# Optimization experiments

Hardware: AMD Instinct MI355X
Metric: run time of the kernel (lower is better)

Reference implementation:

```python
import jax, jax.numpy as jnp
import numpy as np

LPC_ORDER = 32
GAMMA = 1.0  # get_gamma(1, None) == 1


def setup_inputs() -> dict:
    key = jax.random.key(0)
    # PARCOR coefficients, magnitude < 1 for stability; shape (..., M+1)
    k = jax.random.uniform(key, (16, 65536, LPC_ORDER + 1), dtype=jnp.float32)
    return {"k": k}


def reference(k):
    # Levinson-style PARCOR -> LPC recursion (diffsptk par2lpc).
    # a starts as k / gamma; for m = 2..M: a[1:m] += k[m] * flip(a[1:m])
    M1 = k.shape[-1]
    a = k / GAMMA
    for m in range(2, M1):  # fixed, small unrolled loop over order
        km = k[..., m : m + 1]          # (..., 1)  reflection coefficient
        am = a[..., 1:m]                 # (..., m-1) current LPC prefix
        a = a.at[..., 1:m].set(am + km * am[..., ::-1])
    return a
```

## Files before the change

kernel.cpp:

```cpp
#include <hip/hip_runtime.h>

#define M1      33
#define TROWS   64
#define BLK     64
#define TILE_F  (TROWS * M1)
#define PARTIAL 16
#define GRID    2304

__global__ __launch_bounds__(BLK, 1)
void parcor_to_lpc_kernel(const float* __restrict__ k, float* __restrict__ out,
                          int ntiles) {
    __shared__ __align__(16) float lds[2 * TILE_F];
    const int lane = threadIdx.x;

    int tile = blockIdx.x;
    if (tile >= ntiles) return;
    const int stride = gridDim.x;

    float4 R0, R1, R2, R3, R4, R5, R6, R7, R8;

#define LOAD_TILE(gbase)  do {                                        \
        const float4* g4_ = (const float4*)(gbase);                   \
        R0 = g4_[0 * BLK + lane];  R1 = g4_[1 * BLK + lane];          \
        R2 = g4_[2 * BLK + lane];  R3 = g4_[3 * BLK + lane];          \
        R4 = g4_[4 * BLK + lane];  R5 = g4_[5 * BLK + lane];          \
        R6 = g4_[6 * BLK + lane];  R7 = g4_[7 * BLK + lane];          \
        if (lane < PARTIAL) R8 = g4_[8 * BLK + lane];                 \
    } while (0)

#define STAGE_TILE(lbase) do {                                        \
        float4* l4_ = (float4*)(lbase);                               \
        l4_[0 * BLK + lane] = R0;  l4_[1 * BLK + lane] = R1;          \
        l4_[2 * BLK + lane] = R2;  l4_[3 * BLK + lane] = R3;          \
        l4_[4 * BLK + lane] = R4;  l4_[5 * BLK + lane] = R5;          \
        l4_[6 * BLK + lane] = R6;  l4_[7 * BLK + lane] = R7;          \
        if (lane < PARTIAL) l4_[8 * BLK + lane] = R8;                 \
    } while (0)

    LOAD_TILE(k + (size_t)tile * TILE_F);
    STAGE_TILE(lds);

    int buf = 0;
    while (true) {
        const int next = tile + stride;

        if (next < ntiles)
            LOAD_TILE(k + (size_t)next * TILE_F);

        float* L = lds + buf * TILE_F;

        asm volatile("s_waitcnt lgkmcnt(0)" ::: "memory");

        float a[M1];
        #pragma unroll
        for (int j = 0; j < M1; ++j) a[j] = L[lane * M1 + j];

        #pragma unroll
        for (int m = 2; m < M1; ++m) {
            const float km = a[m];
            #pragma unroll
            for (int j = 1; 2 * j < m; ++j) {
                const float x = a[j];
                const float y = a[m - j];
                a[j]     = fmaf(km, y, x);
                a[m - j] = fmaf(km, x, y);
            }
            if ((m & 1) == 0) {
                const int j = m >> 1;
                a[j] = fmaf(km, a[j], a[j]);
            }
        }

        #pragma unroll
        for (int j = 0; j < M1; ++j) L[lane * M1 + j] = a[j];
        asm volatile("s_waitcnt lgkmcnt(0)" ::: "memory");

        {
            const float4* l4 = (const float4*)L;
            float4* g4o = (float4*)(out + (size_t)tile * TILE_F);
            #pragma unroll
            for (int i = 0; i < 8; ++i) g4o[i * BLK + lane] = l4[i * BLK + lane];
            if (lane < PARTIAL) g4o[8 * BLK + lane] = l4[8 * BLK + lane];
        }

        if (next >= ntiles) break;

        STAGE_TILE(lds + (buf ^ 1) * TILE_F);

        tile = next;
        buf ^= 1;
    }
#undef LOAD_TILE
#undef STAGE_TILE
}

__global__ void parcor_to_lpc_tail_kernel(const float* __restrict__ k,
                                          float* __restrict__ out,
                                          int row_start, int nrows) {
    const int row = row_start + blockIdx.x * blockDim.x + threadIdx.x;
    if (row >= nrows) return;
    const float* src = k + (size_t)row * M1;
    float* dst = out + (size_t)row * M1;
    float a[M1];
    #pragma unroll
    for (int j = 0; j < M1; ++j) a[j] = src[j];
    #pragma unroll
    for (int m = 2; m < M1; ++m) {
        const float km = a[m];
        #pragma unroll
        for (int j = 1; 2 * j < m; ++j) {
            const float x = a[j];
            const float y = a[m - j];
            a[j]     = fmaf(km, y, x);
            a[m - j] = fmaf(km, x, y);
        }
        if ((m & 1) == 0) {
            const int j = m >> 1;
            a[j] = fmaf(km, a[j], a[j]);
        }
    }
    #pragma unroll
    for (int j = 0; j < M1; ++j) dst[j] = a[j];
}

extern "C" void kernel_launch(void* const* d_in, const int* in_sizes, int n_in,
                              void* d_out, int out_size, void* d_ws, size_t ws_size,
                              hipStream_t stream) {
    const float* k = (const float*)d_in[0];
    float* out = (float*)d_out;

    const int nrows     = in_sizes[0] / M1;
    const int ntiles    = nrows / TROWS;
    const int tile_rows = ntiles * TROWS;
    const int rem       = nrows - tile_rows;

    if (ntiles > 0) {
        const int grid = ntiles < GRID ? ntiles : GRID;
        parcor_to_lpc_kernel<<<grid, BLK, 0, stream>>>(k, out, ntiles);
    }
    if (rem > 0)
        parcor_to_lpc_tail_kernel<<<(rem + 63) / 64, 64, 0, stream>>>(
            k, out, tile_rows, nrows);
}
```

Measured before the change: 242.8 us.

## Deepen prefetch to two register tile sets with single LDS buffer

Replaces the double-buffered LDS pipeline with two alternating register tile sets (A/B), so global loads are issued two tiles ahead instead of one, while using a single LDS tile buffer. The grid is also resized to 18 blocks per CU times 256. The intent is to keep more memory loads in flight per wave to hide HBM latency in this bandwidth-bound kernel. The cost is doubled register usage for prefetch data, which may lower occupancy or cause spills.

```diff
diff --git a/kernel.cpp b/kernel.cpp
--- a/kernel.cpp
+++ b/kernel.cpp
@@ -5,93 +5,100 @@
 #define BLK     64
 #define TILE_F  (TROWS * M1)
 #define PARTIAL 16
-#define GRID    2304
+#define BPC     18
+#define GRID    (BPC * 256)
 
 __global__ __launch_bounds__(BLK, 1)
 void parcor_to_lpc_kernel(const float* __restrict__ k, float* __restrict__ out,
                           int ntiles) {
-    __shared__ __align__(16) float lds[2 * TILE_F];
+    __shared__ __align__(16) float lds[TILE_F];
     const int lane = threadIdx.x;
 
-    int tile = blockIdx.x;
-    if (tile >= ntiles) return;
-    const int stride = gridDim.x;
+    int tA = blockIdx.x;
+    if (tA >= ntiles) return;
+    const int stride  = gridDim.x;
+    const int stride2 = 2 * stride;
 
-    float4 R0, R1, R2, R3, R4, R5, R6, R7, R8;
+    float4 A0, A1, A2, A3, A4, A5, A6, A7, A8;
+    float4 B0, B1, B2, B3, B4, B5, B6, B7, B8;
 
-#define LOAD_TILE(gbase)  do {                                        \
-        const float4* g4_ = (const float4*)(gbase);                   \
-        R0 = g4_[0 * BLK + lane];  R1 = g4_[1 * BLK + lane];          \
-        R2 = g4_[2 * BLK + lane];  R3 = g4_[3 * BLK + lane];          \
-        R4 = g4_[4 * BLK + lane];  R5 = g4_[5 * BLK + lane];          \
-        R6 = g4_[6 * BLK + lane];  R7 = g4_[7 * BLK + lane];          \
-        if (lane < PARTIAL) R8 = g4_[8 * BLK + lane];                 \
+#define LOADSET(P, gbase) do {                                          \
+        const float4* g4_ = (const float4*)(gbase);                     \
+        P##0 = g4_[0 * BLK + lane];  P##1 = g4_[1 * BLK + lane];        \
+        P##2 = g4_[2 * BLK + lane];  P##3 = g4_[3 * BLK + lane];        \
+        P##4 = g4_[4 * BLK + lane];  P##5 = g4_[5 * BLK + lane];        \
+        P##6 = g4_[6 * BLK + lane];  P##7 = g4_[7 * BLK + lane];        \
+        if (lane < PARTIAL) P##8 = g4_[8 * BLK + lane];                 \
     } while (0)
 
-#define STAGE_TILE(lbase) do {                                        \
-        float4* l4_ = (float4*)(lbase);                               \
-        l4_[0 * BLK + lane] = R0;  l4_[1 * BLK + lane] = R1;          \
-        l4_[2 * BLK + lane] = R2;  l4_[3 * BLK + lane] = R3;          \
-        l4_[4 * BLK + lane] = R4;  l4_[5 * BLK + lane] = R5;          \
-        l4_[6 * BLK + lane] = R6;  l4_[7 * BLK + lane] = R7;          \
-        if (lane < PARTIAL) l4_[8 * BLK + lane] = R8;                 \
+#define STAGESET(P) do {                                                \
+        float4* l4_ = (float4*)lds;                                     \
+        l4_[0 * BLK + lane] = P##0;  l4_[1 * BLK + lane] = P##1;        \
+        l4_[2 * BLK + lane] = P##2;  l4_[3 * BLK + lane] = P##3;        \
+        l4_[4 * BLK + lane] = P##4;  l4_[5 * BLK + lane] = P##5;        \
+        l4_[6 * BLK + lane] = P##6;  l4_[7 * BLK + lane] = P##7;        \
+        if (lane < PARTIAL) l4_[8 * BLK + lane] = P##8;                 \
     } while (0)
 
-    LOAD_TILE(k + (size_t)tile * TILE_F);
-    STAGE_TILE(lds);
+#define PROCESS(tidx) do {                                              \
+        asm volatile("s_waitcnt lgkmcnt(0)" ::: "memory");              \
+        float a[M1];                                                    \
+        _Pragma("unroll")                                               \
+        for (int j = 0; j < M1; ++j) a[j] = lds[lane * M1 + j];         \
+        _Pragma("unroll")                                               \
+        for (int m = 2; m < M1; ++m) {                                  \
+            const float km = a[m];                                      \
+            _Pragma("unroll")                                           \
+            for (int j = 1; 2 * j < m; ++j) {                           \
+                const float x = a[j];                                   \
+                const float y = a[m - j];                               \
+                a[j]     = fmaf(km, y, x);                              \
+                a[m - j] = fmaf(km, x, y);                              \
+            }                                                           \
+            if ((m & 1) == 0) {                                         \
+                const int j_ = m >> 1;                                  \
+                a[j_] = fmaf(km, a[j_], a[j_]);                         \
+            }                                                           \
+        }                                                               \
+        _Pragma("unroll")                                               \
+        for (int j = 0; j < M1; ++j) lds[lane * M1 + j] = a[j];         \
+        asm volatile("s_waitcnt lgkmcnt(0)" ::: "memory");              \
+        const float4* l4_ = (const float4*)lds;                         \
+        float4* g4o_ = (float4*)(out + (size_t)(tidx) * TILE_F);        \
+        _Pragma("unroll")                                               \
+        for (int i = 0; i < 8; ++i)                                     \
+            g4o_[i * BLK + lane] = l4_[i * BLK + lane];                 \
+        if (lane < PARTIAL) g4o_[8 * BLK + lane] = l4_[8 * BLK + lane]; \
+    } while (0)
 
-    int buf = 0;
+    LOADSET(A, k + (size_t)tA * TILE_F);
+    int tB = tA + stride;
+    if (tB < ntiles)
+        LOADSET(B, k + (size_t)tB * TILE_F);
+
     while (true) {
-        const int next = tile + stride;
+        STAGESET(A);
+        {
+            const int tN = tA + stride2;
+            if (tN < ntiles) LOADSET(A, k + (size_t)tN * TILE_F);
+        }
+        PROCESS(tA);
+        if (tB >= ntiles) break;
+        tA += stride2;
 
-        if (next < ntiles)
-            LOAD_TILE(k + (size_t)next * TILE_F);
+        STAGESET(B);
+        {
+            const int tN = tB + stride2;
+            if (tN < ntiles) LOADSET(B, k + (size_t)tN * TILE_F);
+        }
+        PROCESS(tB);
+        if (tA >= ntiles) break;
+        tB += stride2;
+    }
 
-        float* L = lds + buf * TILE_F;
-
-        asm volatile("s_waitcnt lgkmcnt(0)" ::: "memory");
-
-        float a[M1];
-        #pragma unroll
-        for (int j = 0; j < M1; ++j) a[j] = L[lane * M1 + j];
-
-        #pragma unroll
-        for (int m = 2; m < M1; ++m) {
-            const float km = a[m];
-            #pragma unroll
-            for (int j = 1; 2 * j < m; ++j) {
-                const float x = a[j];
-                const float y = a[m - j];
-                a[j]     = fmaf(km, y, x);
-                a[m - j] = fmaf(km, x, y);
-            }
-            if ((m & 1) == 0) {
-                const int j = m >> 1;
-                a[j] = fmaf(km, a[j], a[j]);
-            }
-        }
-
-        #pragma unroll
-        for (int j = 0; j < M1; ++j) L[lane * M1 + j] = a[j];
-        asm volatile("s_waitcnt lgkmcnt(0)" ::: "memory");
-
-        {
-            const float4* l4 = (const float4*)L;
-            float4* g4o = (float4*)(out + (size_t)tile * TILE_F);
-            #pragma unroll
-            for (int i = 0; i < 8; ++i) g4o[i * BLK + lane] = l4[i * BLK + lane];
-            if (lane < PARTIAL) g4o[8 * BLK + lane] = l4[8 * BLK + lane];
-        }
-
-        if (next >= ntiles) break;
-
-        STAGE_TILE(lds + (buf ^ 1) * TILE_F);
-
-        tile = next;
-        buf ^= 1;
-    }
-#undef LOAD_TILE
-#undef STAGE_TILE
+#undef LOADSET
+#undef STAGESET
+#undef PROCESS
 }
 
 __global__ void parcor_to_lpc_tail_kernel(const float* __restrict__ k,
```

Result: no change. 241.2 us (-0.7%).

## Pack four independent waves per block with contiguous tile ranges per wave

Applied to the files above, without the earlier changes.

Blocks go from one wave to four, each wave with its own single LDS tile buffer. Tiles are now split into contiguous per-wave ranges instead of a grid-strided loop, and the grid shrinks to 1024 blocks with launch bounds allowing two blocks per CU. The ninth float4 load is made unconditional by clamping the index, and a scheduling barrier keeps the next tile's prefetch issued before compute. The aim is more resident waves and sequential access per wave, at the cost of dropping LDS double-buffering and possibly uneven work per wave.

```diff
diff --git a/kernel.cpp b/kernel.cpp
--- a/kernel.cpp
+++ b/kernel.cpp
@@ -2,58 +2,66 @@
 
 #define M1      33
 #define TROWS   64
-#define BLK     64
 #define TILE_F  (TROWS * M1)
+#define TILE_V4 528
+#define BLK     256
+#define WPB     4
 #define PARTIAL 16
-#define GRID    2304
+#define GRID    1024
 
-__global__ __launch_bounds__(BLK, 1)
+__global__ __launch_bounds__(BLK, 2)
 void parcor_to_lpc_kernel(const float* __restrict__ k, float* __restrict__ out,
                           int ntiles) {
-    __shared__ __align__(16) float lds[2 * TILE_F];
-    const int lane = threadIdx.x;
+    __shared__ __align__(16) float lds_all[WPB * TILE_F];
+    const int lane = threadIdx.x & 63;
+    const int wid  = threadIdx.x >> 6;
+    float* const lds = lds_all + wid * TILE_F;
 
-    int tile = blockIdx.x;
-    if (tile >= ntiles) return;
-    const int stride = gridDim.x;
+    const int nw  = gridDim.x * WPB;
+    const int gw  = blockIdx.x * WPB + wid;
+    const int tpw = (ntiles + nw - 1) / nw;
+    int t         = gw * tpw;
+    const int t1  = (t + tpw < ntiles) ? t + tpw : ntiles;
+    if (t >= t1) return;
+
+    const int i9 = 8 * TROWS + (lane < PARTIAL ? lane : PARTIAL - 1);
 
     float4 R0, R1, R2, R3, R4, R5, R6, R7, R8;
 
-#define LOAD_TILE(gbase)  do {                                        \
-        const float4* g4_ = (const float4*)(gbase);                   \
-        R0 = g4_[0 * BLK + lane];  R1 = g4_[1 * BLK + lane];          \
-        R2 = g4_[2 * BLK + lane];  R3 = g4_[3 * BLK + lane];          \
-        R4 = g4_[4 * BLK + lane];  R5 = g4_[5 * BLK + lane];          \
-        R6 = g4_[6 * BLK + lane];  R7 = g4_[7 * BLK + lane];          \
-        if (lane < PARTIAL) R8 = g4_[8 * BLK + lane];                 \
+#define LOADSET(tidx) do {                                              \
+        const float4* g4_ = (const float4*)(k + (size_t)(tidx) * TILE_F); \
+        R0 = g4_[0 * TROWS + lane];  R1 = g4_[1 * TROWS + lane];        \
+        R2 = g4_[2 * TROWS + lane];  R3 = g4_[3 * TROWS + lane];        \
+        R4 = g4_[4 * TROWS + lane];  R5 = g4_[5 * TROWS + lane];        \
+        R6 = g4_[6 * TROWS + lane];  R7 = g4_[7 * TROWS + lane];        \
+        R8 = g4_[i9];                                                   \
     } while (0)
 
-#define STAGE_TILE(lbase) do {                                        \
-        float4* l4_ = (float4*)(lbase);                               \
-        l4_[0 * BLK + lane] = R0;  l4_[1 * BLK + lane] = R1;          \
-        l4_[2 * BLK + lane] = R2;  l4_[3 * BLK + lane] = R3;          \
-        l4_[4 * BLK + lane] = R4;  l4_[5 * BLK + lane] = R5;          \
-        l4_[6 * BLK + lane] = R6;  l4_[7 * BLK + lane] = R7;          \
-        if (lane < PARTIAL) l4_[8 * BLK + lane] = R8;                 \
+#define STAGESET() do {                                                 \
+        float4* l4_ = (float4*)lds;                                     \
+        l4_[0 * TROWS + lane] = R0;  l4_[1 * TROWS + lane] = R1;        \
+        l4_[2 * TROWS + lane] = R2;  l4_[3 * TROWS + lane] = R3;        \
+        l4_[4 * TROWS + lane] = R4;  l4_[5 * TROWS + lane] = R5;        \
+        l4_[6 * TROWS + lane] = R6;  l4_[7 * TROWS + lane] = R7;        \
+        if (lane < PARTIAL) l4_[8 * TROWS + lane] = R8;                 \
     } while (0)
 
-    LOAD_TILE(k + (size_t)tile * TILE_F);
-    STAGE_TILE(lds);
+    LOADSET(t);
 
-    int buf = 0;
     while (true) {
-        const int next = tile + stride;
+        STAGESET();
 
-        if (next < ntiles)
-            LOAD_TILE(k + (size_t)next * TILE_F);
-
-        float* L = lds + buf * TILE_F;
+        const int tn = t + 1;
+        if (tn < t1) {
+            LOADSET(tn);
+            __builtin_amdgcn_sched_barrier(0);
+        }
 
         asm volatile("s_waitcnt lgkmcnt(0)" ::: "memory");
 
         float a[M1];
         #pragma unroll
-        for (int j = 0; j < M1; ++j) a[j] = L[lane * M1 + j];
+        for (int j = 0; j < M1; ++j) a[j] = lds[lane * M1 + j];
 
         #pragma unroll
         for (int m = 2; m < M1; ++m) {
@@ -66,32 +74,30 @@
                 a[m - j] = fmaf(km, x, y);
             }
             if ((m & 1) == 0) {
-                const int j = m >> 1;
-                a[j] = fmaf(km, a[j], a[j]);
+                const int jh = m >> 1;
+                a[jh] = fmaf(km, a[jh], a[jh]);
             }
         }
 
         #pragma unroll
-        for (int j = 0; j < M1; ++j) L[lane * M1 + j] = a[j];
+        for (int j = 0; j < M1; ++j) lds[lane * M1 + j] = a[j];
         asm volatile("s_waitcnt lgkmcnt(0)" ::: "memory");
 
         {
-            const float4* l4 = (const float4*)L;
-            float4* g4o = (float4*)(out + (size_t)tile * TILE_F);
+            const float4* l4 = (const float4*)lds;
+            float4* g4o = (float4*)(out + (size_t)t * TILE_F);
             #pragma unroll
-            for (int i = 0; i < 8; ++i) g4o[i * BLK + lane] = l4[i * BLK + lane];
-            if (lane < PARTIAL) g4o[8 * BLK + lane] = l4[8 * BLK + lane];
+            for (int i = 0; i < 8; ++i)
+                g4o[i * TROWS + lane] = l4[i * TROWS + lane];
+            if (lane < PARTIAL)
+                g4o[8 * TROWS + lane] = l4[8 * TROWS + lane];
         }
 
-        if (next >= ntiles) break;
-
-        STAGE_TILE(lds + (buf ^ 1) * TILE_F);
-
-        tile = next;
-        buf ^= 1;
+        if (tn >= t1) break;
+        t = tn;
     }
-#undef LOAD_TILE
-#undef STAGE_TILE
+#undef LOADSET
+#undef STAGESET
 }
 
 __global__ void parcor_to_lpc_tail_kernel(const float* __restrict__ k,
@@ -135,7 +141,8 @@
     const int rem       = nrows - tile_rows;
 
     if (ntiles > 0) {
-        const int grid = ntiles < GRID ? ntiles : GRID;
+        const int grid = (ntiles + WPB - 1) / WPB < GRID
+                       ? (ntiles + WPB - 1) / WPB : GRID;
         parcor_to_lpc_kernel<<<grid, BLK, 0, stream>>>(k, out, ntiles);
     }
     if (rem > 0)
```

New measurement: 241.4 us. No clear change (-0.6%).
